# Kernel tuning notes

Measured on AMD Instinct MI355X. Metric: run time of the kernel, lower is better.

## Reference

```python
import jax, jax.numpy as jnp
import numpy as np

N_NODES = 100000
HIDDEN = 128
N_EDGES = 640000


def setup_inputs() -> dict:
    key = jax.random.key(0)
    ks = jax.random.split(key, 7)
    x = jax.random.normal(ks[0], (N_NODES, HIDDEN), dtype=jnp.float32)
    # torch Linear weights, stored transposed for y = h @ W + b
    W1 = jax.random.normal(ks[1], (HIDDEN, HIDDEN), dtype=jnp.float32) * (1.0 / np.sqrt(HIDDEN))
    b1 = jax.random.normal(ks[2], (HIDDEN,), dtype=jnp.float32) * 0.01
    W2 = jax.random.normal(ks[3], (HIDDEN, 1), dtype=jnp.float32) * (1.0 / np.sqrt(HIDDEN))
    b2 = jax.random.normal(ks[4], (1,), dtype=jnp.float32) * 0.01
    edge_index = jax.random.randint(ks[5], (2, N_EDGES), 0, N_NODES, dtype=jnp.int64 if jax.config.jax_enable_x64 else jnp.int32)
    edge_index_neg = jax.random.randint(ks[6], (2, N_EDGES), 0, N_NODES, dtype=jnp.int64 if jax.config.jax_enable_x64 else jnp.int32)
    return {"x": x, "W1": W1, "b1": b1, "W2": W2, "b2": b2,
            "edge_index": edge_index, "edge_index_neg": edge_index_neg}


def _decode(x, W1, b1, W2, b2, ei):
    # gather endpoints and Hadamard product: [E, hidden]
    h = x[ei[0]] * x[ei[1]]
    # decoder = ReLU -> Linear(h,h) -> ReLU -> Linear(h,1); then sigmoid
    h = jax.nn.relu(h)
    h = jax.nn.relu(h @ W1 + b1)
    return jax.nn.sigmoid(h @ W2 + b2)  # [E, 1]


def reference(x, W1, b1, W2, b2, edge_index, edge_index_neg):
    edge_pos_pred = _decode(x, W1, b1, W2, b2, edge_index)
    edge_neg_pred = _decode(x, W1, b1, W2, b2, edge_index_neg)
    return jnp.concatenate([edge_pos_pred, edge_neg_pred], axis=0)  # [2E, 1]
```

## Files before the change

kernel.cpp:

```cpp
#include <hip/hip_runtime.h>
#include <hip/hip_bf16.h>

#define HID   128
#define PITCH 136
#define TPB   256

typedef __attribute__((ext_vector_type(8)))  __bf16 bf16x8;
typedef __attribute__((ext_vector_type(16))) float  f32x16;

__global__ __launch_bounds__(TPB) void prep_kernel(
    const float* __restrict__ W1, __bf16* __restrict__ w1t,
    const float* __restrict__ x, __bf16* __restrict__ xb, int n_x8) {
  if (xb) {
    for (int i = blockIdx.x * TPB + threadIdx.x; i < n_x8; i += gridDim.x * TPB) {
      float4 a = *reinterpret_cast<const float4*>(x + i * 8);
      float4 b = *reinterpret_cast<const float4*>(x + i * 8 + 4);
      bf16x8 v;
      v[0] = (__bf16)a.x; v[1] = (__bf16)a.y; v[2] = (__bf16)a.z; v[3] = (__bf16)a.w;
      v[4] = (__bf16)b.x; v[5] = (__bf16)b.y; v[6] = (__bf16)b.z; v[7] = (__bf16)b.w;
      *reinterpret_cast<bf16x8*>(xb + i * 8) = v;
    }
  }
  if (blockIdx.x == 0 && w1t) {
    __shared__ float w[HID * HID];
    for (int i = threadIdx.x; i < HID * HID; i += TPB) w[i] = W1[i];
    __syncthreads();
    for (int c = threadIdx.x; c < HID * (HID / 8); c += TPB) {
      int n  = c >> 4;
      int k0 = (c & 15) << 3;
      bf16x8 v;
#pragma unroll
      for (int j = 0; j < 8; ++j) v[j] = (__bf16)w[(k0 + j) * HID + n];
      *reinterpret_cast<bf16x8*>(&w1t[n * PITCH + k0]) = v;
    }
  }
}

__global__ __launch_bounds__(TPB) void vgae_decode_kernel(
    const float* __restrict__ x,
    const __bf16* __restrict__ xb,
    const float* __restrict__ W1,
    const __bf16* __restrict__ w1t,
    const float* __restrict__ b1,
    const float* __restrict__ W2,
    const float* __restrict__ b2,
    const int* __restrict__ eip,
    const int* __restrict__ ein,
    float* __restrict__ out,
    int E, int n_tiles)
{
  __shared__ __bf16 sW[HID * PITCH];
  __shared__ float  sb1[HID];
  __shared__ float  sw2[HID];

  if (w1t) {
    const uint4* srcp = reinterpret_cast<const uint4*>(w1t);
    uint4*       dstp = reinterpret_cast<uint4*>(sW);
    for (int i = threadIdx.x; i < (HID * PITCH) / 8; i += TPB) dstp[i] = srcp[i];
  } else {
    for (int c = threadIdx.x; c < HID * (HID / 8); c += TPB) {
      int n = c >> 4, k0 = (c & 15) << 3;
      bf16x8 v;
#pragma unroll
      for (int j = 0; j < 8; ++j) v[j] = (__bf16)W1[(k0 + j) * HID + n];
      *reinterpret_cast<bf16x8*>(&sW[n * PITCH + k0]) = v;
    }
  }
  if (threadIdx.x < HID) {
    sb1[threadIdx.x] = b1[threadIdx.x];
    sw2[threadIdx.x] = W2[threadIdx.x];
  }
  __syncthreads();

  const int lane = threadIdx.x & 63;
  const int wave = threadIdx.x >> 6;
  const int m    = lane & 31;
  const int half = lane >> 5;
  const float b2v = b2[0];

  int tile = blockIdx.x;
  int nsrc = 0, ndst = 0;
  if (tile < n_tiles) {
    const int e_base = tile * 128 + wave * 32;
    const int* ei = (e_base < E) ? eip : ein;
    const int  eo = (e_base < E) ? e_base : (e_base - E);
    nsrc = ei[eo + m];
    ndst = ei[E + eo + m];
  }

  for (; tile < n_tiles; tile += gridDim.x) {
    const int src = nsrc, dst = ndst;

    const int tn = tile + gridDim.x;
    if (tn < n_tiles) {
      const int e_base = tn * 128 + wave * 32;
      const int* ei = (e_base < E) ? eip : ein;
      const int  eo = (e_base < E) ? e_base : (e_base - E);
      nsrc = ei[eo + m];
      ndst = ei[E + eo + m];
    }

    f32x16 acc[4] = {};

    if (xb) {
      const __bf16* xs = xb + (size_t)src * HID;
      const __bf16* xd = xb + (size_t)dst * HID;
      bf16x8 S[8], D[8];
#pragma unroll
      for (int ks = 0; ks < 8; ++ks) {
        const int k0 = half * 8 + ks * 16;
        S[ks] = *reinterpret_cast<const bf16x8*>(xs + k0);
        D[ks] = *reinterpret_cast<const bf16x8*>(xd + k0);
      }
#pragma unroll
      for (int ks = 0; ks < 8; ++ks) {
        const int k0 = half * 8 + ks * 16;
        bf16x8 a;
#pragma unroll
        for (int j = 0; j < 8; ++j) {
          float p = (float)S[ks][j] * (float)D[ks][j];
          a[j] = (__bf16)fmaxf(p, 0.f);
        }
#pragma unroll
        for (int nt = 0; nt < 4; ++nt) {
          bf16x8 bfr = *reinterpret_cast<const bf16x8*>(&sW[(nt * 32 + m) * PITCH + k0]);
          acc[nt] = __builtin_amdgcn_mfma_f32_32x32x16_bf16(a, bfr, acc[nt], 0, 0, 0);
        }
      }
    } else {
      const float* xs = x + (size_t)src * HID;
      const float* xd = x + (size_t)dst * HID;
#pragma unroll
      for (int ks = 0; ks < 8; ++ks) {
        const int k0 = half * 8 + ks * 16;
        float4 s0 = *reinterpret_cast<const float4*>(xs + k0);
        float4 s1 = *reinterpret_cast<const float4*>(xs + k0 + 4);
        float4 d0 = *reinterpret_cast<const float4*>(xd + k0);
        float4 d1 = *reinterpret_cast<const float4*>(xd + k0 + 4);
        bf16x8 a;
        a[0] = (__bf16)fmaxf(s0.x * d0.x, 0.f);
        a[1] = (__bf16)fmaxf(s0.y * d0.y, 0.f);
        a[2] = (__bf16)fmaxf(s0.z * d0.z, 0.f);
        a[3] = (__bf16)fmaxf(s0.w * d0.w, 0.f);
        a[4] = (__bf16)fmaxf(s1.x * d1.x, 0.f);
        a[5] = (__bf16)fmaxf(s1.y * d1.y, 0.f);
        a[6] = (__bf16)fmaxf(s1.z * d1.z, 0.f);
        a[7] = (__bf16)fmaxf(s1.w * d1.w, 0.f);
#pragma unroll
        for (int nt = 0; nt < 4; ++nt) {
          bf16x8 bfr = *reinterpret_cast<const bf16x8*>(&sW[(nt * 32 + m) * PITCH + k0]);
          acc[nt] = __builtin_amdgcn_mfma_f32_32x32x16_bf16(a, bfr, acc[nt], 0, 0, 0);
        }
      }
    }

    float p[16];
#pragma unroll
    for (int r = 0; r < 16; ++r) p[r] = 0.f;
#pragma unroll
    for (int nt = 0; nt < 4; ++nt) {
      const int n = nt * 32 + m;
      const float b1n = sb1[n];
      const float w2n = sw2[n];
#pragma unroll
      for (int r = 0; r < 16; ++r) {
        float t = fmaxf(acc[nt][r] + b1n, 0.f);
        p[r] = fmaf(t, w2n, p[r]);
      }
    }
#pragma unroll
    for (int off = 1; off < 32; off <<= 1) {
#pragma unroll
      for (int r = 0; r < 16; ++r) p[r] += __shfl_xor(p[r], off, 64);
    }
    if (m < 4) {
      const int g = m;
      float4 o;
      o.x = 1.f / (1.f + __expf(-(p[g * 4 + 0] + b2v)));
      o.y = 1.f / (1.f + __expf(-(p[g * 4 + 1] + b2v)));
      o.z = 1.f / (1.f + __expf(-(p[g * 4 + 2] + b2v)));
      o.w = 1.f / (1.f + __expf(-(p[g * 4 + 3] + b2v)));
      *reinterpret_cast<float4*>(out + tile * 128 + wave * 32 + g * 8 + half * 4) = o;
    }
  }
}

extern "C" void kernel_launch(void* const* d_in, const int* in_sizes, int n_in,
                              void* d_out, int out_size, void* d_ws, size_t ws_size,
                              hipStream_t stream) {
  const float* x  = (const float*)d_in[0];
  const float* W1 = (const float*)d_in[1];
  const float* b1 = (const float*)d_in[2];
  const float* W2 = (const float*)d_in[3];
  const float* b2 = (const float*)d_in[4];
  const int*  eip = (const int*)d_in[5];
  const int*  ein = (const int*)d_in[6];
  float* out = (float*)d_out;
  const int E = in_sizes[5] / 2;
  const int n_tiles = (2 * E) / 128;
  const int n_nodes = in_sizes[0] / HID;
  const int n_x8 = in_sizes[0] / 8;

  const size_t w1t_bytes = (size_t)HID * PITCH * sizeof(__bf16);
  const size_t xb_off    = 65536;
  const size_t xb_bytes  = (size_t)n_nodes * HID * sizeof(__bf16);

  __bf16* w1t = nullptr;
  __bf16* xb  = nullptr;
  if (ws_size >= w1t_bytes) w1t = (__bf16*)d_ws;
  if (ws_size >= xb_off + xb_bytes) xb = (__bf16*)((char*)d_ws + xb_off);

  if (w1t || xb) {
    int prep_grid = xb ? ((n_x8 + TPB - 1) / TPB < 6400 ? (n_x8 + TPB - 1) / TPB : 6400) : 1;
    prep_kernel<<<prep_grid, TPB, 0, stream>>>(W1, w1t, x, xb, n_x8);
  }
  vgae_decode_kernel<<<2560, TPB, 0, stream>>>(x, xb, W1, w1t, b1, W2, b2,
                                               eip, ein, out, E, n_tiles);
}
```

Baseline: 234.6 us.

## Switch decode to 16x16x32 MFMA with 16-edge wave tiles and early gather

The decode kernel now uses the 16x16x32 bf16 MFMA, so each wave handles 16 edges instead of 32, with 8 output-column tiles and 4 K steps. The src/dst row gathers are issued before the next-tile index prefetch. The cross-lane reduction shrinks to 4 shuffle rounds over 4 values instead of 5 rounds over 16. The prep conversion switches to float4-per-thread and the fp32 path moves to a separate fallback kernel, which removes runtime branches from the main kernel. In exchange, each MFMA tile has less reuse and there are twice as many tiles to loop over.

New measurement: 224.7 us. 4.3% less time.

```diff
diff --git a/kernel.cpp b/kernel.cpp
--- a/kernel.cpp
+++ b/kernel.cpp
@@ -5,20 +5,19 @@
 #define PITCH 136
 #define TPB   256
 
-typedef __attribute__((ext_vector_type(8)))  __bf16 bf16x8;
-typedef __attribute__((ext_vector_type(16))) float  f32x16;
+typedef __attribute__((ext_vector_type(8))) __bf16 bf16x8;
+typedef __attribute__((ext_vector_type(4))) __bf16 bf16x4;
+typedef __attribute__((ext_vector_type(4))) float  f32x4;
 
 __global__ __launch_bounds__(TPB) void prep_kernel(
     const float* __restrict__ W1, __bf16* __restrict__ w1t,
-    const float* __restrict__ x, __bf16* __restrict__ xb, int n_x8) {
+    const float* __restrict__ x, __bf16* __restrict__ xb, int n_x4) {
   if (xb) {
-    for (int i = blockIdx.x * TPB + threadIdx.x; i < n_x8; i += gridDim.x * TPB) {
-      float4 a = *reinterpret_cast<const float4*>(x + i * 8);
-      float4 b = *reinterpret_cast<const float4*>(x + i * 8 + 4);
-      bf16x8 v;
+    for (int i = blockIdx.x * TPB + threadIdx.x; i < n_x4; i += gridDim.x * TPB) {
+      float4 a = reinterpret_cast<const float4*>(x)[i];
+      bf16x4 v;
       v[0] = (__bf16)a.x; v[1] = (__bf16)a.y; v[2] = (__bf16)a.z; v[3] = (__bf16)a.w;
-      v[4] = (__bf16)b.x; v[5] = (__bf16)b.y; v[6] = (__bf16)b.z; v[7] = (__bf16)b.w;
-      *reinterpret_cast<bf16x8*>(xb + i * 8) = v;
+      reinterpret_cast<bf16x4*>(xb)[i] = v;
     }
   }
   if (blockIdx.x == 0 && w1t) {
@@ -37,9 +36,7 @@
 }
 
 __global__ __launch_bounds__(TPB) void vgae_decode_kernel(
-    const float* __restrict__ x,
     const __bf16* __restrict__ xb,
-    const float* __restrict__ W1,
     const __bf16* __restrict__ w1t,
     const float* __restrict__ b1,
     const float* __restrict__ W2,
@@ -53,18 +50,10 @@
   __shared__ float  sb1[HID];
   __shared__ float  sw2[HID];
 
-  if (w1t) {
+  {
     const uint4* srcp = reinterpret_cast<const uint4*>(w1t);
     uint4*       dstp = reinterpret_cast<uint4*>(sW);
     for (int i = threadIdx.x; i < (HID * PITCH) / 8; i += TPB) dstp[i] = srcp[i];
-  } else {
-    for (int c = threadIdx.x; c < HID * (HID / 8); c += TPB) {
-      int n = c >> 4, k0 = (c & 15) << 3;
-      bf16x8 v;
-#pragma unroll
-      for (int j = 0; j < 8; ++j) v[j] = (__bf16)W1[(k0 + j) * HID + n];
-      *reinterpret_cast<bf16x8*>(&sW[n * PITCH + k0]) = v;
-    }
   }
   if (threadIdx.x < HID) {
     sb1[threadIdx.x] = b1[threadIdx.x];
@@ -74,14 +63,14 @@
 
   const int lane = threadIdx.x & 63;
   const int wave = threadIdx.x >> 6;
-  const int m    = lane & 31;
-  const int half = lane >> 5;
+  const int m    = lane & 15;
+  const int quad = lane >> 4;
   const float b2v = b2[0];
 
   int tile = blockIdx.x;
   int nsrc = 0, ndst = 0;
   if (tile < n_tiles) {
-    const int e_base = tile * 128 + wave * 32;
+    const int e_base = tile * 64 + wave * 16;
     const int* ei = (e_base < E) ? eip : ein;
     const int  eo = (e_base < E) ? e_base : (e_base - E);
     nsrc = ei[eo + m];
@@ -90,97 +79,143 @@
 
   for (; tile < n_tiles; tile += gridDim.x) {
     const int src = nsrc, dst = ndst;
+    const __bf16* xs = xb + (size_t)src * HID;
+    const __bf16* xd = xb + (size_t)dst * HID;
+
+    bf16x8 S[4], D[4];
+#pragma unroll
+    for (int kt = 0; kt < 4; ++kt) {
+      const int k0 = kt * 32 + quad * 8;
+      S[kt] = *reinterpret_cast<const bf16x8*>(xs + k0);
+      D[kt] = *reinterpret_cast<const bf16x8*>(xd + k0);
+    }
 
     const int tn = tile + gridDim.x;
     if (tn < n_tiles) {
-      const int e_base = tn * 128 + wave * 32;
+      const int e_base = tn * 64 + wave * 16;
       const int* ei = (e_base < E) ? eip : ein;
       const int  eo = (e_base < E) ? e_base : (e_base - E);
       nsrc = ei[eo + m];
       ndst = ei[E + eo + m];
     }
 
-    f32x16 acc[4] = {};
-
-    if (xb) {
-      const __bf16* xs = xb + (size_t)src * HID;
-      const __bf16* xd = xb + (size_t)dst * HID;
-      bf16x8 S[8], D[8];
-#pragma unroll
-      for (int ks = 0; ks < 8; ++ks) {
-        const int k0 = half * 8 + ks * 16;
-        S[ks] = *reinterpret_cast<const bf16x8*>(xs + k0);
-        D[ks] = *reinterpret_cast<const bf16x8*>(xd + k0);
-      }
-#pragma unroll
-      for (int ks = 0; ks < 8; ++ks) {
-        const int k0 = half * 8 + ks * 16;
-        bf16x8 a;
-#pragma unroll
-        for (int j = 0; j < 8; ++j) {
-          float p = (float)S[ks][j] * (float)D[ks][j];
-          a[j] = (__bf16)fmaxf(p, 0.f);
-        }
-#pragma unroll
-        for (int nt = 0; nt < 4; ++nt) {
-          bf16x8 bfr = *reinterpret_cast<const bf16x8*>(&sW[(nt * 32 + m) * PITCH + k0]);
-          acc[nt] = __builtin_amdgcn_mfma_f32_32x32x16_bf16(a, bfr, acc[nt], 0, 0, 0);
-        }
-      }
-    } else {
-      const float* xs = x + (size_t)src * HID;
-      const float* xd = x + (size_t)dst * HID;
-#pragma unroll
-      for (int ks = 0; ks < 8; ++ks) {
-        const int k0 = half * 8 + ks * 16;
-        float4 s0 = *reinterpret_cast<const float4*>(xs + k0);
-        float4 s1 = *reinterpret_cast<const float4*>(xs + k0 + 4);
-        float4 d0 = *reinterpret_cast<const float4*>(xd + k0);
-        float4 d1 = *reinterpret_cast<const float4*>(xd + k0 + 4);
-        bf16x8 a;
-        a[0] = (__bf16)fmaxf(s0.x * d0.x, 0.f);
-        a[1] = (__bf16)fmaxf(s0.y * d0.y, 0.f);
-        a[2] = (__bf16)fmaxf(s0.z * d0.z, 0.f);
-        a[3] = (__bf16)fmaxf(s0.w * d0.w, 0.f);
-        a[4] = (__bf16)fmaxf(s1.x * d1.x, 0.f);
-        a[5] = (__bf16)fmaxf(s1.y * d1.y, 0.f);
-        a[6] = (__bf16)fmaxf(s1.z * d1.z, 0.f);
-        a[7] = (__bf16)fmaxf(s1.w * d1.w, 0.f);
-#pragma unroll
-        for (int nt = 0; nt < 4; ++nt) {
-          bf16x8 bfr = *reinterpret_cast<const bf16x8*>(&sW[(nt * 32 + m) * PITCH + k0]);
-          acc[nt] = __builtin_amdgcn_mfma_f32_32x32x16_bf16(a, bfr, acc[nt], 0, 0, 0);
-        }
-      }
-    }
-
-    float p[16];
-#pragma unroll
-    for (int r = 0; r < 16; ++r) p[r] = 0.f;
-#pragma unroll
-    for (int nt = 0; nt < 4; ++nt) {
-      const int n = nt * 32 + m;
+    f32x4 acc[8] = {};
+
+#pragma unroll
+    for (int kt = 0; kt < 4; ++kt) {
+      const int k0 = kt * 32 + quad * 8;
+      bf16x8 a;
+#pragma unroll
+      for (int j = 0; j < 8; ++j) {
+        float p = (float)S[kt][j] * (float)D[kt][j];
+        a[j] = (__bf16)fmaxf(p, 0.f);
+      }
+#pragma unroll
+      for (int nt = 0; nt < 8; ++nt) {
+        bf16x8 bfr = *reinterpret_cast<const bf16x8*>(&sW[(nt * 16 + m) * PITCH + k0]);
+        acc[nt] = __builtin_amdgcn_mfma_f32_16x16x32_bf16(a, bfr, acc[nt], 0, 0, 0);
+      }
+    }
+
+    float p[4] = {0.f, 0.f, 0.f, 0.f};
+#pragma unroll
+    for (int nt = 0; nt < 8; ++nt) {
+      const int n = nt * 16 + m;
       const float b1n = sb1[n];
       const float w2n = sw2[n];
 #pragma unroll
-      for (int r = 0; r < 16; ++r) {
+      for (int r = 0; r < 4; ++r) {
         float t = fmaxf(acc[nt][r] + b1n, 0.f);
         p[r] = fmaf(t, w2n, p[r]);
       }
     }
 #pragma unroll
-    for (int off = 1; off < 32; off <<= 1) {
-#pragma unroll
-      for (int r = 0; r < 16; ++r) p[r] += __shfl_xor(p[r], off, 64);
-    }
-    if (m < 4) {
-      const int g = m;
+    for (int off = 1; off < 16; off <<= 1) {
+#pragma unroll
+      for (int r = 0; r < 4; ++r) p[r] += __shfl_xor(p[r], off, 64);
+    }
+    if (m == 0) {
       float4 o;
-      o.x = 1.f / (1.f + __expf(-(p[g * 4 + 0] + b2v)));
-      o.y = 1.f / (1.f + __expf(-(p[g * 4 + 1] + b2v)));
-      o.z = 1.f / (1.f + __expf(-(p[g * 4 + 2] + b2v)));
-      o.w = 1.f / (1.f + __expf(-(p[g * 4 + 3] + b2v)));
-      *reinterpret_cast<float4*>(out + tile * 128 + wave * 32 + g * 8 + half * 4) = o;
+      o.x = 1.f / (1.f + __expf(-(p[0] + b2v)));
+      o.y = 1.f / (1.f + __expf(-(p[1] + b2v)));
+      o.z = 1.f / (1.f + __expf(-(p[2] + b2v)));
+      o.w = 1.f / (1.f + __expf(-(p[3] + b2v)));
+      *reinterpret_cast<float4*>(out + tile * 64 + wave * 16 + quad * 4) = o;
+    }
+  }
+}
+
+__global__ __launch_bounds__(TPB) void vgae_decode_fallback(
+    const float* __restrict__ x,
+    const float* __restrict__ W1,
+    const float* __restrict__ b1,
+    const float* __restrict__ W2,
+    const float* __restrict__ b2,
+    const int* __restrict__ eip,
+    const int* __restrict__ ein,
+    float* __restrict__ out,
+    int E, int n_tiles)
+{
+  __shared__ __bf16 sW[HID * PITCH];
+  __shared__ float  sb1[HID];
+  __shared__ float  sw2[HID];
+  for (int c = threadIdx.x; c < HID * (HID / 8); c += TPB) {
+    int n = c >> 4, k0 = (c & 15) << 3;
+    bf16x8 v;
+#pragma unroll
+    for (int j = 0; j < 8; ++j) v[j] = (__bf16)W1[(k0 + j) * HID + n];
+    *reinterpret_cast<bf16x8*>(&sW[n * PITCH + k0]) = v;
+  }
+  if (threadIdx.x < HID) { sb1[threadIdx.x] = b1[threadIdx.x]; sw2[threadIdx.x] = W2[threadIdx.x]; }
+  __syncthreads();
+  const int lane = threadIdx.x & 63, wave = threadIdx.x >> 6;
+  const int m = lane & 15, quad = lane >> 4;
+  const float b2v = b2[0];
+  for (int tile = blockIdx.x; tile < n_tiles; tile += gridDim.x) {
+    const int e_base = tile * 64 + wave * 16;
+    const int* ei = (e_base < E) ? eip : ein;
+    const int  eo = (e_base < E) ? e_base : (e_base - E);
+    const int src = ei[eo + m], dst = ei[E + eo + m];
+    const float* xs = x + (size_t)src * HID;
+    const float* xd = x + (size_t)dst * HID;
+    f32x4 acc[8] = {};
+#pragma unroll
+    for (int kt = 0; kt < 4; ++kt) {
+      const int k0 = kt * 32 + quad * 8;
+      float4 s0 = *reinterpret_cast<const float4*>(xs + k0);
+      float4 s1 = *reinterpret_cast<const float4*>(xs + k0 + 4);
+      float4 d0 = *reinterpret_cast<const float4*>(xd + k0);
+      float4 d1 = *reinterpret_cast<const float4*>(xd + k0 + 4);
+      bf16x8 a;
+      a[0] = (__bf16)fmaxf(s0.x * d0.x, 0.f); a[1] = (__bf16)fmaxf(s0.y * d0.y, 0.f);
+      a[2] = (__bf16)fmaxf(s0.z * d0.z, 0.f); a[3] = (__bf16)fmaxf(s0.w * d0.w, 0.f);
+      a[4] = (__bf16)fmaxf(s1.x * d1.x, 0.f); a[5] = (__bf16)fmaxf(s1.y * d1.y, 0.f);
+      a[6] = (__bf16)fmaxf(s1.z * d1.z, 0.f); a[7] = (__bf16)fmaxf(s1.w * d1.w, 0.f);
+#pragma unroll
+      for (int nt = 0; nt < 8; ++nt) {
+        bf16x8 bfr = *reinterpret_cast<const bf16x8*>(&sW[(nt * 16 + m) * PITCH + k0]);
+        acc[nt] = __builtin_amdgcn_mfma_f32_16x16x32_bf16(a, bfr, acc[nt], 0, 0, 0);
+      }
+    }
+    float p[4] = {0.f, 0.f, 0.f, 0.f};
+#pragma unroll
+    for (int nt = 0; nt < 8; ++nt) {
+      const int n = nt * 16 + m;
+      const float b1n = sb1[n], w2n = sw2[n];
+#pragma unroll
+      for (int r = 0; r < 4; ++r) p[r] = fmaf(fmaxf(acc[nt][r] + b1n, 0.f), w2n, p[r]);
+    }
+#pragma unroll
+    for (int off = 1; off < 16; off <<= 1)
+#pragma unroll
+      for (int r = 0; r < 4; ++r) p[r] += __shfl_xor(p[r], off, 64);
+    if (m == 0) {
+      float4 o;
+      o.x = 1.f / (1.f + __expf(-(p[0] + b2v)));
+      o.y = 1.f / (1.f + __expf(-(p[1] + b2v)));
+      o.z = 1.f / (1.f + __expf(-(p[2] + b2v)));
+      o.w = 1.f / (1.f + __expf(-(p[3] + b2v)));
+      *reinterpret_cast<float4*>(out + tile * 64 + wave * 16 + quad * 4) = o;
     }
   }
 }
@@ -197,9 +232,9 @@
   const int*  ein = (const int*)d_in[6];
   float* out = (float*)d_out;
   const int E = in_sizes[5] / 2;
-  const int n_tiles = (2 * E) / 128;
+  const int n_tiles = (2 * E) / 64;
   const int n_nodes = in_sizes[0] / HID;
-  const int n_x8 = in_sizes[0] / 8;
+  const int n_x4 = in_sizes[0] / 4;
 
   const size_t w1t_bytes = (size_t)HID * PITCH * sizeof(__bf16);
   const size_t xb_off    = 65536;
@@ -210,10 +245,14 @@
   if (ws_size >= w1t_bytes) w1t = (__bf16*)d_ws;
   if (ws_size >= xb_off + xb_bytes) xb = (__bf16*)((char*)d_ws + xb_off);
 
-  if (w1t || xb) {
-    int prep_grid = xb ? ((n_x8 + TPB - 1) / TPB < 6400 ? (n_x8 + TPB - 1) / TPB : 6400) : 1;
-    prep_kernel<<<prep_grid, TPB, 0, stream>>>(W1, w1t, x, xb, n_x8);
-  }
-  vgae_decode_kernel<<<2560, TPB, 0, stream>>>(x, xb, W1, w1t, b1, W2, b2,
-                                               eip, ein, out, E, n_tiles);
-}
+  if (w1t && xb) {
+    int prep_grid = (n_x4 + TPB - 1) / TPB;
+    if (prep_grid > 6400) prep_grid = 6400;
+    prep_kernel<<<prep_grid, TPB, 0, stream>>>(W1, w1t, x, xb, n_x4);
+    vgae_decode_kernel<<<2560, TPB, 0, stream>>>(xb, w1t, b1, W2, b2,
+                                                 eip, ein, out, E, n_tiles);
+  } else {
+    vgae_decode_fallback<<<2560, TPB, 0, stream>>>(x, W1, b1, W2, b2,
+                                                   eip, ein, out, E, n_tiles);
+  }
+}
```
